# Performance work log

Hardware: AMD Instinct MI355X
Metric: run time of the kernel (lower is better)

## Reference

```python
import jax, jax.numpy as jnp
import numpy as np

N_NODES = 100000
N_EDGES = 3200000
IN_CH = 256


def setup_inputs() -> dict:
    key = jax.random.key(0)
    ks = jax.random.split(key, 8)
    x = jax.random.normal(ks[0], (N_NODES, IN_CH), dtype=jnp.float32)
    edge_index = jax.random.randint(ks[1], (2, N_EDGES), 0, N_NODES, dtype=jnp.int64)
    alpha = jnp.ones((), dtype=jnp.float32)
    beta = jnp.ones((), dtype=jnp.float32)
    s = 1.0 / np.sqrt(IN_CH)
    W_mlp = jax.random.normal(ks[2], (1, IN_CH), dtype=jnp.float32) * s
    W_lin = jax.random.normal(ks[3], (1, IN_CH), dtype=jnp.float32) * s
    W_gcn = jax.random.normal(ks[4], (1, IN_CH), dtype=jnp.float32) * s
    W_att = jax.random.normal(ks[5], (3, 3), dtype=jnp.float32) * (1.0 / np.sqrt(3))
    b_att = jax.random.normal(ks[6], (3,), dtype=jnp.float32) * 0.1
    return {"x": x, "edge_index": edge_index, "alpha": alpha, "beta": beta,
            "W_mlp": W_mlp, "W_lin": W_lin, "W_gcn": W_gcn,
            "W_att": W_att, "b_att": b_att}


def _gcn_conv(x, edge_index, W_gcn, num_nodes):
    # PyG GCNConv: add self-loops, symmetric normalization, no bias.
    loop = jnp.arange(num_nodes, dtype=edge_index.dtype)
    row = jnp.concatenate([edge_index[0], loop])  # source
    col = jnp.concatenate([edge_index[1], loop])  # target
    deg = jax.ops.segment_sum(jnp.ones_like(col, dtype=x.dtype), col,
                              num_segments=num_nodes)
    dinv = jnp.where(deg > 0, jax.lax.rsqrt(deg), 0.0)
    norm = dinv[row] * dinv[col]                  # [E+N]
    xw = x @ W_gcn.T                               # [N, 1]
    msg = norm[:, None] * xw[row]                  # [E+N, 1]
    return jax.ops.segment_sum(msg, col, num_segments=num_nodes)  # [N, 1]


def reference(x, edge_index, alpha, beta, W_mlp, W_lin, W_gcn, W_att, b_att):
    num_nodes = x.shape[0]
    # score1: in-degree based
    deg = jax.ops.segment_sum(jnp.ones((edge_index.shape[1],), dtype=x.dtype),
                              edge_index[1], num_segments=num_nodes)
    score1 = jax.nn.sigmoid(alpha * jnp.sqrt(deg) + beta)           # [N]
    # score2: tiny MLP
    score2 = jax.nn.sigmoid((x @ W_mlp.T)[:, 0])                    # [N]
    # score3: GCNConv + linear
    gcn_out = _gcn_conv(x, edge_index, W_gcn, num_nodes)            # [N,1]
    score3 = jax.nn.sigmoid((gcn_out + x @ W_lin.T)[:, 0])          # [N]
    scores = jnp.stack([score1, score2, score3], axis=1)            # [N,3]
    weight = jax.nn.softmax(scores @ W_att.T + b_att, axis=1)       # [N,3]
    fitness = jnp.sum(weight * scores, axis=1)                      # [N]
    return fitness
```

## Files before the change

kernel.cpp:

```cpp
#include <hip/hip_runtime.h>
#include <math.h>

#define N_CH    256
#define SBSHIFT 11
#define SBN     2048
#define NSMAX   64
#define CH      4096

__device__ __forceinline__ float sigmoidf_(float v) {
    return 1.0f / (1.0f + expf(-v));
}

__device__ __forceinline__ void build_tables(const int* sbT, int ns,
                                             int* sbsL, int* cstL) {
    if (threadIdx.x == 0) {
        int run = 0, c = 0;
        for (int i = 0; i < ns; ++i) {
            sbsL[i] = run;
            cstL[i] = c;
            int len = sbT[i];
            run += len;
            c += (len + CH - 1) / CH;
        }
        sbsL[ns] = run;
        cstL[ns] = c;
    }
}

__global__ __launch_bounds__(256) void dots_hist_kernel(
    const float* __restrict__ x,
    const float* __restrict__ Wmlp, const float* __restrict__ Wlin,
    const float* __restrict__ Wgcn, const int* __restrict__ dst,
    float* __restrict__ s2dot, float* __restrict__ s3lin, float* __restrict__ xw,
    int* __restrict__ H1,
    int n_nodes, int n_edges, int ns, int nch)
{
    __shared__ int h8[NSMAX * 8];
    if ((int)blockIdx.x < nch) {
        int c = blockIdx.x;
        for (int i = threadIdx.x; i < NSMAX * 8; i += 256) h8[i] = 0;
        __syncthreads();
        int copy = (int)threadIdx.x & 7;
        int start = c * CH;
        #pragma unroll
        for (int m = 0; m < 4; ++m) {
            int e = start + (m * 256 + (int)threadIdx.x) * 4;
            if (e + 3 < n_edges) {
                int4 d4 = *(const int4*)(dst + e);
                atomicAdd(&h8[(d4.x >> SBSHIFT) * 8 + copy], 1);
                atomicAdd(&h8[(d4.y >> SBSHIFT) * 8 + copy], 1);
                atomicAdd(&h8[(d4.z >> SBSHIFT) * 8 + copy], 1);
                atomicAdd(&h8[(d4.w >> SBSHIFT) * 8 + copy], 1);
            } else {
                for (int ee = e; ee < n_edges && ee >= 0; ++ee)
                    atomicAdd(&h8[(dst[ee] >> SBSHIFT) * 8 + copy], 1);
            }
        }
        __syncthreads();
        if (threadIdx.x < (unsigned)ns) {
            int s = 0;
            #pragma unroll
            for (int k = 0; k < 8; ++k) s += h8[threadIdx.x * 8 + k];
            H1[(size_t)threadIdx.x * nch + c] = s;
        }
        return;
    }

    int wid  = ((int)blockIdx.x - nch) * 4 + ((int)threadIdx.x >> 6);
    int lane = threadIdx.x & 63;
    if (wid >= n_nodes) return;

    const float4* xr = (const float4*)(x + (size_t)wid * N_CH);
    float4 v  = xr[lane];
    float4 wm = ((const float4*)Wmlp)[lane];
    float4 wl = ((const float4*)Wlin)[lane];
    float4 wg = ((const float4*)Wgcn)[lane];

    float d0 = v.x*wm.x + v.y*wm.y + v.z*wm.z + v.w*wm.w;
    float d1 = v.x*wl.x + v.y*wl.y + v.z*wl.z + v.w*wl.w;
    float d2 = v.x*wg.x + v.y*wg.y + v.z*wg.z + v.w*wg.w;

    #pragma unroll
    for (int off = 32; off; off >>= 1) {
        d0 += __shfl_down(d0, off, 64);
        d1 += __shfl_down(d1, off, 64);
        d2 += __shfl_down(d2, off, 64);
    }
    if (lane == 0) { s2dot[wid] = d0; s3lin[wid] = d1; xw[wid] = d2; }
}

__global__ __launch_bounds__(1024) void scanA_kernel(
    const int* __restrict__ H1, int* __restrict__ O, int* __restrict__ sbT,
    int nch)
{
    __shared__ int s[1024];
    int sb = blockIdx.x, t = threadIdx.x;
    int v = (t < nch) ? H1[(size_t)sb * nch + t] : 0;
    s[t] = v;
    __syncthreads();
    for (int off = 1; off < 1024; off <<= 1) {
        int a = s[t];
        int b = (t >= off) ? s[t - off] : 0;
        __syncthreads();
        s[t] = a + b;
        __syncthreads();
    }
    if (t < nch) O[(size_t)sb * nch + t] = s[t] - v;
    if (t == 1023) sbT[sb] = s[1023];
}

__global__ __launch_bounds__(256) void scatter_kernel(
    const int* __restrict__ src, const int* __restrict__ dst,
    const int* __restrict__ sbT, const int* __restrict__ O,
    const int* __restrict__ H1,
    int* __restrict__ cpack, int n_edges, int ns, int nch)
{
    __shared__ int lp[NSMAX + 1];
    __shared__ int dl[NSMAX];
    __shared__ int h2[NSMAX];
    __shared__ unsigned short sbOf[CH];
    __shared__ int sorted[CH];

    int c = blockIdx.x;
    int t = threadIdx.x;

    if (t < 64) {
        h2[t] = 0;
        int hv = (t < ns) ? H1[(size_t)t * nch + c] : 0;
        int sv = (t < ns) ? sbT[t] : 0;
        int hi = hv, si = sv;
        #pragma unroll
        for (int off = 1; off < 64; off <<= 1) {
            int a = __shfl_up(hi, off, 64); if (t >= off) hi += a;
            int b = __shfl_up(si, off, 64); if (t >= off) si += b;
        }
        if (t < ns) {
            int lpe = hi - hv;
            lp[t] = lpe;
            int sbs = si - sv;
            dl[t] = sbs + O[(size_t)t * nch + c] - lpe;
        }
        if (t == ns - 1) lp[ns] = hi;
    }
    __syncthreads();

    if (t < ns) {
        int p0 = lp[t], p1 = lp[t + 1];
        for (int p = p0; p < p1; ++p) sbOf[p] = (unsigned short)t;
    }

    int start = c * CH;
    int cnt = n_edges - start; if (cnt > CH) cnt = CH;

    #pragma unroll
    for (int m = 0; m < 4; ++m) {
        int e = start + (m * 256 + t) * 4;
        if (e + 3 < n_edges) {
            int4 s4 = *(const int4*)(src + e);
            int4 d4 = *(const int4*)(dst + e);
            int sb, r;
            sb = d4.x >> SBSHIFT; r = atomicAdd(&h2[sb], 1);
            sorted[lp[sb] + r] = s4.x | ((d4.x & (SBN - 1)) << 17);
            sb = d4.y >> SBSHIFT; r = atomicAdd(&h2[sb], 1);
            sorted[lp[sb] + r] = s4.y | ((d4.y & (SBN - 1)) << 17);
            sb = d4.z >> SBSHIFT; r = atomicAdd(&h2[sb], 1);
            sorted[lp[sb] + r] = s4.z | ((d4.z & (SBN - 1)) << 17);
            sb = d4.w >> SBSHIFT; r = atomicAdd(&h2[sb], 1);
            sorted[lp[sb] + r] = s4.w | ((d4.w & (SBN - 1)) << 17);
        } else {
            for (int j = 0; j < 4; ++j) {
                int ee = e + j;
                if (ee < n_edges && ee >= 0) {
                    int sv = src[ee], dv = dst[ee];
                    int sb = dv >> SBSHIFT;
                    int r = atomicAdd(&h2[sb], 1);
                    sorted[lp[sb] + r] = sv | ((dv & (SBN - 1)) << 17);
                }
            }
        }
    }
    __syncthreads();

    for (int p = t; p < cnt; p += 256) {
        cpack[dl[sbOf[p]] + p] = sorted[p];
    }
}

__global__ __launch_bounds__(256) void chunkDeg_kernel(
    const int* __restrict__ cpack, const int* __restrict__ sbT,
    int* __restrict__ partialD, int ns)
{
    __shared__ int sbsL[NSMAX + 1], cstL[NSMAX + 1];
    __shared__ int cnt[SBN];
    build_tables(sbT, ns, sbsL, cstL);
    for (int i = threadIdx.x; i < SBN; i += 256) cnt[i] = 0;
    __syncthreads();
    int c = blockIdx.x;
    if (c >= cstL[ns]) return;
    int lo = 0, hi = ns;
    while (hi - lo > 1) { int mid = (lo + hi) >> 1; if (cstL[mid] <= c) lo = mid; else hi = mid; }
    int sb = lo;
    int i0 = c - cstL[sb];
    int base = sbsL[sb] + i0 * CH;
    int len = sbsL[sb + 1] - base; if (len > CH) len = CH;

    #pragma unroll
    for (int m = 0; m < 4; ++m) {
        int e = (m * 256 + (int)threadIdx.x) * 4;
        if (e + 3 < len) {
            int4 w4 = *(const int4*)(cpack + base + e);
            atomicAdd(&cnt[w4.x >> 17], 1);
            atomicAdd(&cnt[w4.y >> 17], 1);
            atomicAdd(&cnt[w4.z >> 17], 1);
            atomicAdd(&cnt[w4.w >> 17], 1);
        } else {
            for (int ee = e; ee < len && ee >= 0; ++ee)
                atomicAdd(&cnt[cpack[base + ee] >> 17], 1);
        }
    }
    __syncthreads();
    int* row = partialD + (size_t)c * SBN;
    for (int i = threadIdx.x; i < SBN; i += 256) row[i] = cnt[i];
}

__global__ __launch_bounds__(256) void reduceDeg_kernel(
    const int* __restrict__ partialD, const int* __restrict__ sbT,
    const float* __restrict__ xw,
    float* __restrict__ degf, float* __restrict__ dinv, float* __restrict__ sxw,
    int n_nodes, int ns)
{
    __shared__ int sbsL[NSMAX + 1], cstL[NSMAX + 1];
    build_tables(sbT, ns, sbsL, cstL);
    __syncthreads();
    int i = blockIdx.x * 256 + threadIdx.x;
    if (i >= n_nodes) return;
    int sb = i >> SBSHIFT, li = i & (SBN - 1);
    int c0 = cstL[sb], c1 = cstL[sb + 1];
    int d = 0;
    for (int c = c0; c < c1; ++c) d += partialD[(size_t)c * SBN + li];
    float df = (float)d;
    degf[i] = df;
    float di = rsqrtf(df + 1.0f);
    dinv[i] = di;
    sxw[i]  = di * xw[i];
}

__global__ __launch_bounds__(256) void chunkAcc_kernel(
    const int* __restrict__ cpack, const int* __restrict__ sbT,
    const float* __restrict__ sxw, float* __restrict__ partialF, int ns)
{
    __shared__ int sbsL[NSMAX + 1], cstL[NSMAX + 1];
    __shared__ float facc[SBN];
    build_tables(sbT, ns, sbsL, cstL);
    for (int i = threadIdx.x; i < SBN; i += 256) facc[i] = 0.0f;
    __syncthreads();
    int c = blockIdx.x;
    if (c >= cstL[ns]) return;
    int lo = 0, hi = ns;
    while (hi - lo > 1) { int mid = (lo + hi) >> 1; if (cstL[mid] <= c) lo = mid; else hi = mid; }
    int sb = lo;
    int i0 = c - cstL[sb];
    int base = sbsL[sb] + i0 * CH;
    int len = sbsL[sb + 1] - base; if (len > CH) len = CH;

    #pragma unroll
    for (int m = 0; m < 4; ++m) {
        int e = (m * 256 + (int)threadIdx.x) * 4;
        if (e + 3 < len) {
            int4 w4 = *(const int4*)(cpack + base + e);
            atomicAdd(&facc[w4.x >> 17], sxw[w4.x & 0x1FFFF]);
            atomicAdd(&facc[w4.y >> 17], sxw[w4.y & 0x1FFFF]);
            atomicAdd(&facc[w4.z >> 17], sxw[w4.z & 0x1FFFF]);
            atomicAdd(&facc[w4.w >> 17], sxw[w4.w & 0x1FFFF]);
        } else {
            for (int ee = e; ee < len && ee >= 0; ++ee) {
                int w = cpack[base + ee];
                atomicAdd(&facc[w >> 17], sxw[w & 0x1FFFF]);
            }
        }
    }
    __syncthreads();
    float* row = partialF + (size_t)c * SBN;
    for (int i = threadIdx.x; i < SBN; i += 256) row[i] = facc[i];
}

__global__ __launch_bounds__(256) void reduceFinal_kernel(
    const float* __restrict__ partialF, const int* __restrict__ sbT,
    const float* __restrict__ degf, const float* __restrict__ dinv,
    const float* __restrict__ xw, const float* __restrict__ s2dot,
    const float* __restrict__ s3lin,
    const float* __restrict__ alpha, const float* __restrict__ beta,
    const float* __restrict__ Watt, const float* __restrict__ batt,
    float* __restrict__ out, int n_nodes, int ns)
{
    __shared__ int sbsL[NSMAX + 1], cstL[NSMAX + 1];
    build_tables(sbT, ns, sbsL, cstL);
    __syncthreads();
    int i = blockIdx.x * 256 + threadIdx.x;
    if (i >= n_nodes) return;
    int sb = i >> SBSHIFT, li = i & (SBN - 1);
    int c0 = cstL[sb], c1 = cstL[sb + 1];
    float acc = 0.0f;
    for (int c = c0; c < c1; ++c) acc += partialF[(size_t)c * SBN + li];

    float dn = dinv[i];
    float g  = acc * dn + dn * dn * xw[i];
    float s1 = sigmoidf_(alpha[0] * sqrtf(degf[i]) + beta[0]);
    float s2 = sigmoidf_(s2dot[i]);
    float s3 = sigmoidf_(g + s3lin[i]);

    float z0 = Watt[0]*s1 + Watt[1]*s2 + Watt[2]*s3 + batt[0];
    float z1 = Watt[3]*s1 + Watt[4]*s2 + Watt[5]*s3 + batt[1];
    float z2 = Watt[6]*s1 + Watt[7]*s2 + Watt[8]*s3 + batt[2];

    float m  = fmaxf(z0, fmaxf(z1, z2));
    float e0 = expf(z0 - m), e1 = expf(z1 - m), e2 = expf(z2 - m);
    float inv = 1.0f / (e0 + e1 + e2);
    out[i] = (e0 * s1 + e1 * s2 + e2 * s3) * inv;
}

extern "C" void kernel_launch(void* const* d_in, const int* in_sizes, int n_in,
                              void* d_out, int out_size, void* d_ws, size_t ws_size,
                              hipStream_t stream) {
    const float* x     = (const float*)d_in[0];
    const int*   ei    = (const int*)d_in[1];
    const float* alpha = (const float*)d_in[2];
    const float* beta  = (const float*)d_in[3];
    const float* Wmlp  = (const float*)d_in[4];
    const float* Wlin  = (const float*)d_in[5];
    const float* Wgcn  = (const float*)d_in[6];
    const float* Watt  = (const float*)d_in[7];
    const float* batt  = (const float*)d_in[8];
    float* out = (float*)d_out;

    int n_nodes = in_sizes[0] / N_CH;
    int n_edges = in_sizes[1] / 2;
    const int* src = ei;
    const int* dst = ei + n_edges;

    int ns  = (n_nodes + SBN - 1) >> SBSHIFT;
    int nch = (n_edges + CH - 1) / CH;
    int maxChunks = nch + ns;

    size_t off = 0;
    int*   cpack    = (int*)d_ws;          off += (((size_t)n_edges + 1023) & ~(size_t)1023);
    int*   H1       = (int*)d_ws + off;    off += (((size_t)ns * nch + 1023) & ~(size_t)1023);
    int*   O        = (int*)d_ws + off;    off += (((size_t)ns * nch + 1023) & ~(size_t)1023);
    int*   sbT      = (int*)d_ws + off;    off += 128;
    int*   partialD = (int*)d_ws + off;    off += (size_t)maxChunks * SBN;
    float* partialF = (float*)d_ws + off;  off += (size_t)maxChunks * SBN;
    float* s2dot    = (float*)d_ws + off;  off += (((size_t)n_nodes + 1023) & ~(size_t)1023);
    float* s3lin    = (float*)d_ws + off;  off += (((size_t)n_nodes + 1023) & ~(size_t)1023);
    float* xw       = (float*)d_ws + off;  off += (((size_t)n_nodes + 1023) & ~(size_t)1023);
    float* degf     = (float*)d_ws + off;  off += (((size_t)n_nodes + 1023) & ~(size_t)1023);
    float* dinv     = (float*)d_ws + off;  off += (((size_t)n_nodes + 1023) & ~(size_t)1023);
    float* sxw      = (float*)d_ws + off;  off += (((size_t)n_nodes + 1023) & ~(size_t)1023);

    int dotsBlocks = (n_nodes + 3) / 4;
    dots_hist_kernel<<<nch + dotsBlocks, 256, 0, stream>>>(
        x, Wmlp, Wlin, Wgcn, dst, s2dot, s3lin, xw, H1,
        n_nodes, n_edges, ns, nch);

    scanA_kernel<<<ns, 1024, 0, stream>>>(H1, O, sbT, nch);

    scatter_kernel<<<nch, 256, 0, stream>>>(src, dst, sbT, O, H1, cpack,
                                            n_edges, ns, nch);

    chunkDeg_kernel<<<maxChunks, 256, 0, stream>>>(cpack, sbT, partialD, ns);

    reduceDeg_kernel<<<(n_nodes + 255) / 256, 256, 0, stream>>>(
        partialD, sbT, xw, degf, dinv, sxw, n_nodes, ns);

    chunkAcc_kernel<<<maxChunks, 256, 0, stream>>>(cpack, sbT, sxw, partialF, ns);

    reduceFinal_kernel<<<(n_nodes + 255) / 256, 256, 0, stream>>>(
        partialF, sbT, degf, dinv, xw, s2dot, s3lin,
        alpha, beta, Watt, batt, out, n_nodes, ns);
}
```

Measured before the change: 232.4 us.

## Fuse per-superblock reductions into chunk kernels via last-block-done counters

Merges the degree reduction into the chunk-degree kernel and the final score reduction into the chunk-accumulate kernel. Each chunk block atomically increments a per-superblock done counter, and the last block to finish reduces that superblock's partial rows. This drops two kernel launches and the gaps between them. In exchange the final reduction for each superblock runs in a single block, which may serialize work, and the change adds a memset and threadfence costs.

```diff
diff --git a/kernel.cpp b/kernel.cpp
--- a/kernel.cpp
+++ b/kernel.cpp
@@ -6,6 +6,7 @@
 #define SBN     2048
 #define NSMAX   64
 #define CH      4096
+
 
 __device__ __forceinline__ float sigmoidf_(float v) {
     return 1.0f / (1.0f + expf(-v));
@@ -186,27 +187,32 @@
     }
 }
 
-__global__ __launch_bounds__(256) void chunkDeg_kernel(
+__global__ __launch_bounds__(256) void chunkDegRed_kernel(
     const int* __restrict__ cpack, const int* __restrict__ sbT,
-    int* __restrict__ partialD, int ns)
+    const float* __restrict__ xw,
+    int* __restrict__ partialD, int* __restrict__ doneD,
+    float* __restrict__ degf, float* __restrict__ dinv, float* __restrict__ sxw,
+    int n_nodes, int ns)
 {
     __shared__ int sbsL[NSMAX + 1], cstL[NSMAX + 1];
     __shared__ int cnt[SBN];
+    __shared__ int lastFlag;
     build_tables(sbT, ns, sbsL, cstL);
     for (int i = threadIdx.x; i < SBN; i += 256) cnt[i] = 0;
     __syncthreads();
     int c = blockIdx.x;
+    int t = threadIdx.x;
     if (c >= cstL[ns]) return;
     int lo = 0, hi = ns;
     while (hi - lo > 1) { int mid = (lo + hi) >> 1; if (cstL[mid] <= c) lo = mid; else hi = mid; }
     int sb = lo;
-    int i0 = c - cstL[sb];
-    int base = sbsL[sb] + i0 * CH;
+    int c0 = cstL[sb], c1 = cstL[sb + 1];
+    int base = sbsL[sb] + (c - c0) * CH;
     int len = sbsL[sb + 1] - base; if (len > CH) len = CH;
 
     #pragma unroll
     for (int m = 0; m < 4; ++m) {
-        int e = (m * 256 + (int)threadIdx.x) * 4;
+        int e = (m * 256 + t) * 4;
         if (e + 3 < len) {
             int4 w4 = *(const int4*)(cpack + base + e);
             atomicAdd(&cnt[w4.x >> 17], 1);
@@ -220,52 +226,62 @@
     }
     __syncthreads();
     int* row = partialD + (size_t)c * SBN;
-    for (int i = threadIdx.x; i < SBN; i += 256) row[i] = cnt[i];
-}
-
-__global__ __launch_bounds__(256) void reduceDeg_kernel(
-    const int* __restrict__ partialD, const int* __restrict__ sbT,
-    const float* __restrict__ xw,
-    float* __restrict__ degf, float* __restrict__ dinv, float* __restrict__ sxw,
-    int n_nodes, int ns)
-{
-    __shared__ int sbsL[NSMAX + 1], cstL[NSMAX + 1];
-    build_tables(sbT, ns, sbsL, cstL);
-    __syncthreads();
-    int i = blockIdx.x * 256 + threadIdx.x;
-    if (i >= n_nodes) return;
-    int sb = i >> SBSHIFT, li = i & (SBN - 1);
-    int c0 = cstL[sb], c1 = cstL[sb + 1];
-    int d = 0;
-    for (int c = c0; c < c1; ++c) d += partialD[(size_t)c * SBN + li];
-    float df = (float)d;
-    degf[i] = df;
-    float di = rsqrtf(df + 1.0f);
-    dinv[i] = di;
-    sxw[i]  = di * xw[i];
-}
-
-__global__ __launch_bounds__(256) void chunkAcc_kernel(
+    for (int i = t; i < SBN; i += 256) row[i] = cnt[i];
+
+    __threadfence();
+    __syncthreads();
+    if (t == 0) {
+        int old = atomicAdd(&doneD[sb], 1);
+        lastFlag = (old == (c1 - c0 - 1));
+    }
+    __syncthreads();
+    if (!lastFlag) return;
+    __threadfence();
+
+    int i0 = sb << SBSHIFT;
+    for (int li = t; li < SBN; li += 256) {
+        int i = i0 + li;
+        if (i >= n_nodes) continue;
+        int d = 0;
+        for (int cc = c0; cc < c1; ++cc) d += partialD[(size_t)cc * SBN + li];
+        float df = (float)d;
+        degf[i] = df;
+        float di = rsqrtf(df + 1.0f);
+        dinv[i] = di;
+        sxw[i]  = di * xw[i];
+    }
+}
+
+__global__ __launch_bounds__(256) void chunkAccFin_kernel(
     const int* __restrict__ cpack, const int* __restrict__ sbT,
-    const float* __restrict__ sxw, float* __restrict__ partialF, int ns)
+    const float* __restrict__ sxw, float* __restrict__ partialF,
+    int* __restrict__ doneA,
+    const float* __restrict__ degf, const float* __restrict__ dinv,
+    const float* __restrict__ xw, const float* __restrict__ s2dot,
+    const float* __restrict__ s3lin,
+    const float* __restrict__ alpha, const float* __restrict__ beta,
+    const float* __restrict__ Watt, const float* __restrict__ batt,
+    float* __restrict__ out, int n_nodes, int ns)
 {
     __shared__ int sbsL[NSMAX + 1], cstL[NSMAX + 1];
     __shared__ float facc[SBN];
+    __shared__ int lastFlag;
     build_tables(sbT, ns, sbsL, cstL);
     for (int i = threadIdx.x; i < SBN; i += 256) facc[i] = 0.0f;
     __syncthreads();
     int c = blockIdx.x;
+    int t = threadIdx.x;
     if (c >= cstL[ns]) return;
     int lo = 0, hi = ns;
     while (hi - lo > 1) { int mid = (lo + hi) >> 1; if (cstL[mid] <= c) lo = mid; else hi = mid; }
     int sb = lo;
-    int i0 = c - cstL[sb];
-    int base = sbsL[sb] + i0 * CH;
+    int c0 = cstL[sb], c1 = cstL[sb + 1];
+    int base = sbsL[sb] + (c - c0) * CH;
     int len = sbsL[sb + 1] - base; if (len > CH) len = CH;
 
     #pragma unroll
     for (int m = 0; m < 4; ++m) {
-        int e = (m * 256 + (int)threadIdx.x) * 4;
+        int e = (m * 256 + t) * 4;
         if (e + 3 < len) {
             int4 w4 = *(const int4*)(cpack + base + e);
             atomicAdd(&facc[w4.x >> 17], sxw[w4.x & 0x1FFFF]);
@@ -281,42 +297,41 @@
     }
     __syncthreads();
     float* row = partialF + (size_t)c * SBN;
-    for (int i = threadIdx.x; i < SBN; i += 256) row[i] = facc[i];
-}
-
-__global__ __launch_bounds__(256) void reduceFinal_kernel(
-    const float* __restrict__ partialF, const int* __restrict__ sbT,
-    const float* __restrict__ degf, const float* __restrict__ dinv,
-    const float* __restrict__ xw, const float* __restrict__ s2dot,
-    const float* __restrict__ s3lin,
-    const float* __restrict__ alpha, const float* __restrict__ beta,
-    const float* __restrict__ Watt, const float* __restrict__ batt,
-    float* __restrict__ out, int n_nodes, int ns)
-{
-    __shared__ int sbsL[NSMAX + 1], cstL[NSMAX + 1];
-    build_tables(sbT, ns, sbsL, cstL);
-    __syncthreads();
-    int i = blockIdx.x * 256 + threadIdx.x;
-    if (i >= n_nodes) return;
-    int sb = i >> SBSHIFT, li = i & (SBN - 1);
-    int c0 = cstL[sb], c1 = cstL[sb + 1];
-    float acc = 0.0f;
-    for (int c = c0; c < c1; ++c) acc += partialF[(size_t)c * SBN + li];
-
-    float dn = dinv[i];
-    float g  = acc * dn + dn * dn * xw[i];
-    float s1 = sigmoidf_(alpha[0] * sqrtf(degf[i]) + beta[0]);
-    float s2 = sigmoidf_(s2dot[i]);
-    float s3 = sigmoidf_(g + s3lin[i]);
-
-    float z0 = Watt[0]*s1 + Watt[1]*s2 + Watt[2]*s3 + batt[0];
-    float z1 = Watt[3]*s1 + Watt[4]*s2 + Watt[5]*s3 + batt[1];
-    float z2 = Watt[6]*s1 + Watt[7]*s2 + Watt[8]*s3 + batt[2];
-
-    float m  = fmaxf(z0, fmaxf(z1, z2));
-    float e0 = expf(z0 - m), e1 = expf(z1 - m), e2 = expf(z2 - m);
-    float inv = 1.0f / (e0 + e1 + e2);
-    out[i] = (e0 * s1 + e1 * s2 + e2 * s3) * inv;
+    for (int i = t; i < SBN; i += 256) row[i] = facc[i];
+
+    __threadfence();
+    __syncthreads();
+    if (t == 0) {
+        int old = atomicAdd(&doneA[sb], 1);
+        lastFlag = (old == (c1 - c0 - 1));
+    }
+    __syncthreads();
+    if (!lastFlag) return;
+    __threadfence();
+
+    float a0 = alpha[0], b0 = beta[0];
+    int i0 = sb << SBSHIFT;
+    for (int li = t; li < SBN; li += 256) {
+        int i = i0 + li;
+        if (i >= n_nodes) continue;
+        float acc = 0.0f;
+        for (int cc = c0; cc < c1; ++cc) acc += partialF[(size_t)cc * SBN + li];
+
+        float dn = dinv[i];
+        float g  = acc * dn + dn * dn * xw[i];
+        float s1 = sigmoidf_(a0 * sqrtf(degf[i]) + b0);
+        float s2 = sigmoidf_(s2dot[i]);
+        float s3 = sigmoidf_(g + s3lin[i]);
+
+        float z0 = Watt[0]*s1 + Watt[1]*s2 + Watt[2]*s3 + batt[0];
+        float z1 = Watt[3]*s1 + Watt[4]*s2 + Watt[5]*s3 + batt[1];
+        float z2 = Watt[6]*s1 + Watt[7]*s2 + Watt[8]*s3 + batt[2];
+
+        float m  = fmaxf(z0, fmaxf(z1, z2));
+        float e0 = expf(z0 - m), e1 = expf(z1 - m), e2 = expf(z2 - m);
+        float inv = 1.0f / (e0 + e1 + e2);
+        out[i] = (e0 * s1 + e1 * s2 + e2 * s3) * inv;
+    }
 }
 
 extern "C" void kernel_launch(void* const* d_in, const int* in_sizes, int n_in,
@@ -347,6 +362,8 @@
     int*   H1       = (int*)d_ws + off;    off += (((size_t)ns * nch + 1023) & ~(size_t)1023);
     int*   O        = (int*)d_ws + off;    off += (((size_t)ns * nch + 1023) & ~(size_t)1023);
     int*   sbT      = (int*)d_ws + off;    off += 128;
+    int*   doneD    = (int*)d_ws + off;    off += 64;
+    int*   doneA    = (int*)d_ws + off;    off += 64;
     int*   partialD = (int*)d_ws + off;    off += (size_t)maxChunks * SBN;
     float* partialF = (float*)d_ws + off;  off += (size_t)maxChunks * SBN;
     float* s2dot    = (float*)d_ws + off;  off += (((size_t)n_nodes + 1023) & ~(size_t)1023);
@@ -356,6 +373,8 @@
     float* dinv     = (float*)d_ws + off;  off += (((size_t)n_nodes + 1023) & ~(size_t)1023);
     float* sxw      = (float*)d_ws + off;  off += (((size_t)n_nodes + 1023) & ~(size_t)1023);
 
+    hipMemsetAsync(doneD, 0, 128 * sizeof(int), stream);
+
     int dotsBlocks = (n_nodes + 3) / 4;
     dots_hist_kernel<<<nch + dotsBlocks, 256, 0, stream>>>(
         x, Wmlp, Wlin, Wgcn, dst, s2dot, s3lin, xw, H1,
@@ -366,14 +385,11 @@
     scatter_kernel<<<nch, 256, 0, stream>>>(src, dst, sbT, O, H1, cpack,
                                             n_edges, ns, nch);
 
-    chunkDeg_kernel<<<maxChunks, 256, 0, stream>>>(cpack, sbT, partialD, ns);
-
-    reduceDeg_kernel<<<(n_nodes + 255) / 256, 256, 0, stream>>>(
-        partialD, sbT, xw, degf, dinv, sxw, n_nodes, ns);
-
-    chunkAcc_kernel<<<maxChunks, 256, 0, stream>>>(cpack, sbT, sxw, partialF, ns);
-
-    reduceFinal_kernel<<<(n_nodes + 255) / 256, 256, 0, stream>>>(
-        partialF, sbT, degf, dinv, xw, s2dot, s3lin,
+    chunkDegRed_kernel<<<maxChunks, 256, 0, stream>>>(
+        cpack, sbT, xw, partialD, doneD, degf, dinv, sxw, n_nodes, ns);
+
+    chunkAccFin_kernel<<<maxChunks, 256, 0, stream>>>(
+        cpack, sbT, sxw, partialF, doneA,
+        degf, dinv, xw, s2dot, s3lin,
         alpha, beta, Watt, batt, out, n_nodes, ns);
 }
```

New measurement: 461.9 us. 98.8% more time.
